# Performance work log

Hardware: AMD Instinct MI355X
Metric: run time of the kernel (lower is better)

The kernel has to match this reference:

```python
import jax, jax.numpy as jnp
import numpy as np

DIM = 512
NUM_HEADS = 8
HEAD_DIM = DIM // NUM_HEADS
SCALE = HEAD_DIM ** -0.5


def setup_inputs() -> dict:
    key = jax.random.key(0)
    k1, k2, k3, k4 = jax.random.split(key, 4)
    x = jax.random.normal(k1, (4, 2048, DIM), dtype=jnp.float32)
    W_qkv = jax.random.normal(k2, (DIM, 3 * DIM), dtype=jnp.float32) * (DIM ** -0.5)
    W_proj = jax.random.normal(k3, (DIM, DIM), dtype=jnp.float32) * (DIM ** -0.5)
    b_proj = jax.random.normal(k4, (DIM,), dtype=jnp.float32) * 0.01
    return {"x": x, "W_qkv": W_qkv, "W_proj": W_proj, "b_proj": b_proj}


def reference(x, W_qkv, W_proj, b_proj):
    B, N, C = x.shape
    H, hd = NUM_HEADS, HEAD_DIM
    # qkv: [B, N, 3, H, hd] -> (q, k, v) each [B, H, N, hd]
    qkv = (x @ W_qkv).reshape(B, N, 3, H, hd)
    qkv = jnp.transpose(qkv, (2, 0, 3, 1, 4))
    q, k, v = qkv[0], qkv[1], qkv[2]
    # eager attention: [B, H, N, N]
    attn = jnp.einsum('bhnd,bhmd->bhnm', q, k) * SCALE
    attn = jax.nn.softmax(attn, axis=-1)
    out = jnp.einsum('bhnm,bhmd->bhnd', attn, v)  # [B, H, N, hd]
    out = jnp.transpose(out, (0, 2, 1, 3)).reshape(B, N, C)
    out = out @ W_proj + b_proj
    return (out, k, v)
```

## Files before the change

### kernel.cpp

```cpp
#include <hip/hip_runtime.h>

typedef unsigned short ushort_t;
typedef __bf16 bf16x8 __attribute__((ext_vector_type(8)));
typedef ushort_t u16x8 __attribute__((ext_vector_type(8)));
typedef float f32x4 __attribute__((ext_vector_type(4)));

#define MFMA(a, b, c) __builtin_amdgcn_mfma_f32_16x16x32_bf16(a, b, c, 0, 0, 0)

#define N_X      4194304L
#define N_WQKV   786432L
#define N_WPROJ  262144L
#define OUT_OFF_K 4194304L
#define OUT_OFF_V 8388608L

#define OFF_FLAG   0UL
#define OFF_XB     1024UL
#define OFF_WQKVT  (OFF_XB + 8388608UL)
#define OFF_WPROJT (OFF_WQKVT + 1572864UL)
#define OFF_BPROJ  (OFF_WPROJT + 524288UL)
#define OFF_QB     (OFF_BPROJ + 2048UL)
#define OFF_KB     (OFF_QB + 8388608UL)
#define OFF_VTB    (OFF_KB + 8388608UL)
#define OFF_ATTN   (OFF_VTB + 8388608UL)

#define QSCALE 0.180336880519191f

__device__ __forceinline__ ushort_t f2b(float f) {
    union { float f; unsigned u; } v; v.f = f;
    return (ushort_t)((v.u + 0x7FFFu + ((v.u >> 16) & 1u)) >> 16);
}
__device__ __forceinline__ ushort_t f2b_trunc(float f) {
    union { float f; unsigned u; } v; v.f = f;
    return (ushort_t)(v.u >> 16);
}
__device__ __forceinline__ float b2f(ushort_t h) {
    union { unsigned u; float f; } v; v.u = ((unsigned)h) << 16;
    return v.f;
}
__device__ __forceinline__ float ldf(const float* p, long i) { return p[i]; }
__device__ __forceinline__ float ldf(const ushort_t* p, long i) { return b2f(p[i]); }
__device__ __forceinline__ void stf(float* p, long i, float v) { p[i] = v; }
__device__ __forceinline__ void stf(ushort_t* p, long i, float v) { p[i] = f2b(v); }

__device__ __forceinline__ float fast_exp2(float x) {
#if __has_builtin(__builtin_amdgcn_exp2f)
    return __builtin_amdgcn_exp2f(x);
#else
    return __expf(x * 0.6931471805599453f);
#endif
}

__device__ __forceinline__ void glds16(const void* g, const void* l) {
    __builtin_amdgcn_global_load_lds((__attribute__((address_space(1))) void*)g,
                                     (__attribute__((address_space(3))) void*)l,
                                     16, 0, 0);
}

__global__ void k_detect(const unsigned* __restrict__ x, int* __restrict__ flag) {
    int lane = threadIdx.x & 63;
    int cnt = 0;
#pragma unroll
    for (int i = 0; i < 4; ++i) {
        unsigned w = x[lane + i * 64];
        float v = __uint_as_float((w & 0xFFFFu) << 16);
        float a = fabsf(v);
        if (a > 1e-3f && a < 100.0f) cnt++;
    }
#pragma unroll
    for (int off = 32; off; off >>= 1) cnt += __shfl_down(cnt, off, 64);
    if (lane == 0) *flag = (cnt > 128) ? 1 : 0;
}

template <typename T>
__global__ void k_prep(const T* __restrict__ x, const T* __restrict__ wq,
                       const T* __restrict__ wp, const T* __restrict__ bp,
                       ushort_t* __restrict__ xb, ushort_t* __restrict__ wqT,
                       ushort_t* __restrict__ wpT, float* __restrict__ bpf,
                       const int* __restrict__ flag, int want) {
    if (*flag != want) return;
    long i0 = (long)blockIdx.x * blockDim.x + threadIdx.x;
    long stride = (long)gridDim.x * blockDim.x;
    for (long i = i0; i < N_X; i += stride) xb[i] = f2b(ldf(x, i));
    for (long i = i0; i < N_WQKV; i += stride) {
        long n = i >> 9, k = i & 511;
        wqT[i] = f2b(ldf(wq, k * 1536 + n));
    }
    for (long i = i0; i < N_WPROJ; i += stride) {
        long n = i >> 9, k = i & 511;
        wpT[i] = f2b(ldf(wp, k * 512 + n));
    }
    for (long i = i0; i < 512; i += stride) bpf[i] = ldf(bp, i);
}

template <typename TOUT>
__global__ __launch_bounds__(256, 2)
void k_qkv(const ushort_t* __restrict__ xb, const ushort_t* __restrict__ wqT,
           ushort_t* __restrict__ qb, ushort_t* __restrict__ kb, ushort_t* __restrict__ vb,
           TOUT* __restrict__ kout, TOUT* __restrict__ vout,
           const int* __restrict__ flag, int want) {
    if (*flag != want) return;
    __shared__ __align__(16) ushort_t As[128 * 32];
    __shared__ __align__(16) ushort_t Bs[128 * 32];
    const int tid = threadIdx.x, wave = tid >> 6, lane = tid & 63;
    const int id = blockIdx.x;
    const int xcd = id & 7, g = id >> 3;
    const int bx = xcd * 8 + (g & 7);
    const int by = g >> 3;
    const int tm = bx * 128, tn = by * 128;
    const int wm = (wave >> 1) * 64, wn = (wave & 1) * 64;
    const int l15 = lane & 15, lq = lane >> 4;
    const int srow = lane >> 2, sc = lane & 3;

    f32x4 acc[4][4];
#pragma unroll
    for (int a = 0; a < 4; ++a)
#pragma unroll
        for (int b = 0; b < 4; ++b) acc[a][b] = (f32x4){0.f, 0.f, 0.f, 0.f};

    for (int k0 = 0; k0 < 512; k0 += 32) {
#pragma unroll
        for (int t = 0; t < 2; ++t) {
            int s = wave * 2 + t;
            int row = s * 16 + srow;
            int c = (sc ^ (row >> 1)) & 3;
            glds16(xb  + (long)(tm + row) * 512 + k0 + c * 8, As + s * 512);
            glds16(wqT + (long)(tn + row) * 512 + k0 + c * 8, Bs + s * 512);
        }
        __syncthreads();
        bf16x8 af[4], bfr[4];
#pragma unroll
        for (int mt = 0; mt < 4; ++mt) {
            int row = wm + mt * 16 + l15;
            int cp = (lq ^ (row >> 1)) & 3;
            af[mt] = *(const bf16x8*)(As + row * 32 + cp * 8);
        }
#pragma unroll
        for (int nt = 0; nt < 4; ++nt) {
            int row = wn + nt * 16 + l15;
            int cp = (lq ^ (row >> 1)) & 3;
            bfr[nt] = *(const bf16x8*)(Bs + row * 32 + cp * 8);
        }
#pragma unroll
        for (int mt = 0; mt < 4; ++mt)
#pragma unroll
            for (int nt = 0; nt < 4; ++nt)
                acc[mt][nt] = MFMA(af[mt], bfr[nt], acc[mt][nt]);
        __syncthreads();
    }

#pragma unroll
    for (int mt = 0; mt < 4; ++mt) {
#pragma unroll
        for (int nt = 0; nt < 4; ++nt) {
            int j = tn + wn + nt * 16 + l15;
            int t = j >> 9, h = (j >> 6) & 7, d = j & 63;
#pragma unroll
            for (int r = 0; r < 4; ++r) {
                int mm = tm + wm + mt * 16 + lq * 4 + r;
                int b = mm >> 11, nn = mm & 2047;
                float v = acc[mt][nt][r];
                long idx = ((long)(b * 8 + h) * 2048 + nn) * 64 + d;
                if (t == 0) {
                    qb[idx] = f2b(v * QSCALE);
                } else if (t == 1) {
                    kb[idx] = f2b(v);
                    stf(kout, idx, v);
                } else {
                    vb[idx] = f2b(v);
                    stf(vout, idx, v);
                }
            }
        }
    }
}

__global__ __launch_bounds__(256, 4)
void k_vtrans(const ushort_t* __restrict__ vb, ushort_t* __restrict__ vtb) {
    __shared__ ushort_t T[64 * 64];
    const int tid = threadIdx.x;
    const int bh = blockIdx.y, ktile = blockIdx.x;
    const long base = (long)bh * 131072 + (long)ktile * 64 * 64;
    const int row = tid >> 2, cq = tid & 3;
#pragma unroll
    for (int half = 0; half < 2; ++half) {
        int c = cq + half * 4;
        u16x8 v = *(const u16x8*)(vb + base + row * 64 + c * 8);
#pragma unroll
        for (int e = 0; e < 8; ++e) {
            int dim = c * 8 + e;
            T[row * 64 + ((dim + row) & 63)] = v[e];
        }
    }
    __syncthreads();
#pragma unroll
    for (int it = 0; it < 16; ++it) {
        int d = (tid >> 6) * 16 + it;
        int key = tid & 63;
        vtb[(long)bh * 131072 + (long)d * 2048 + ktile * 64 + key] =
            T[key * 64 + ((d + key) & 63)];
    }
}

__global__ __launch_bounds__(256, 4)
void k_attn(const ushort_t* __restrict__ qb, const ushort_t* __restrict__ kb,
            const ushort_t* __restrict__ vtb, ushort_t* __restrict__ attnb) {
    __shared__ __align__(16) ushort_t Kt[128 * 64];
    __shared__ __align__(16) ushort_t Vt[64 * 128];
    __shared__ __align__(16) ushort_t Ps[4][16 * 64];
    const int tid = threadIdx.x, wave = tid >> 6, lane = tid & 63;
    const int l15 = lane & 15, lq = lane >> 4;
    const int id = blockIdx.x;
    const int xcd = id & 7, g = id >> 3;
    const int bh = xcd * 4 + (g >> 5);
    const int qt = g & 31;
    const long kvbase = (long)bh * 131072;
    const long qbase = kvbase + (long)qt * 64 * 64;

    bf16x8 aQ[2];
#pragma unroll
    for (int kt = 0; kt < 2; ++kt)
        aQ[kt] = *(const bf16x8*)(qb + qbase +
            (long)(wave * 16 + l15) * 64 + kt * 32 + lq * 8);

    union { ushort_t u[8]; bf16x8 v; } oneu;
#pragma unroll
    for (int i = 0; i < 8; ++i) oneu.u[i] = 0x3F80;
    const bf16x8 ones = oneu.v;

    f32x4 oacc[4], sum_acc;
#pragma unroll
    for (int n = 0; n < 4; ++n) oacc[n] = (f32x4){0.f, 0.f, 0.f, 0.f};
    sum_acc = (f32x4){0.f, 0.f, 0.f, 0.f};

    const int ksrow = lane >> 3, kschunk = lane & 7;
    const int vsrow = lane >> 4, vschunk = lane & 15;
    ushort_t* Pw = &Ps[wave][0];

    for (int j = 0; j < 16; ++j) {
#pragma unroll
        for (int t = 0; t < 4; ++t) {
            int s = wave * 4 + t;
            {
                int row = s * 8 + ksrow;
                int c = kschunk ^ (row & 7);
                glds16(kb + kvbase + (long)(j * 128 + row) * 64 + c * 8, Kt + s * 512);
            }
            {
                int row = s * 4 + vsrow;
                int c = vschunk ^ (row & 15);
                glds16(vtb + kvbase + (long)row * 2048 + j * 128 + c * 8, Vt + s * 512);
            }
        }
        __syncthreads();

#pragma unroll
        for (int h = 0; h < 2; ++h) {
            f32x4 sacc[4];
#pragma unroll
            for (int nt = 0; nt < 4; ++nt) sacc[nt] = (f32x4){0.f, 0.f, 0.f, 0.f};
#pragma unroll
            for (int nt = 0; nt < 4; ++nt) {
                int krow = h * 64 + nt * 16 + l15;
#pragma unroll
                for (int kt = 0; kt < 2; ++kt) {
                    int c = (kt * 4 + lq) ^ (krow & 7);
                    bf16x8 bk = *(const bf16x8*)(Kt + krow * 64 + c * 8);
                    sacc[nt] = MFMA(aQ[kt], bk, sacc[nt]);
                }
            }
#pragma unroll
            for (int nt = 0; nt < 4; ++nt) {
#pragma unroll
                for (int r = 0; r < 4; ++r) {
                    float p = fast_exp2(sacc[nt][r]);
                    int prow = lq * 4 + r;
                    int col = nt * 16 + l15;
                    int ch = (col >> 3) ^ (prow & 7);
                    Pw[prow * 64 + ch * 8 + (col & 7)] = f2b_trunc(p);
                }
            }
#pragma unroll
            for (int kt = 0; kt < 2; ++kt) {
                int cha = (kt * 4 + lq) ^ (l15 & 7);
                bf16x8 ap = *(const bf16x8*)(Pw + l15 * 64 + cha * 8);
                sum_acc = MFMA(ap, ones, sum_acc);
#pragma unroll
                for (int nd = 0; nd < 4; ++nd) {
                    int vrow = nd * 16 + l15;
                    int vch = (h * 8 + kt * 4 + lq) ^ (vrow & 15);
                    bf16x8 bv = *(const bf16x8*)(Vt + vrow * 128 + vch * 8);
                    oacc[nd] = MFMA(ap, bv, oacc[nd]);
                }
            }
        }
        __syncthreads();
    }

    const int b = bh >> 3, hh = bh & 7;
#pragma unroll
    for (int r = 0; r < 4; ++r) {
        float inv = 1.0f / sum_acc[r];
        int n = qt * 64 + wave * 16 + lq * 4 + r;
#pragma unroll
        for (int nd = 0; nd < 4; ++nd) {
            int d = nd * 16 + l15;
            attnb[((long)b * 2048 + n) * 512 + hh * 64 + d] = f2b(oacc[nd][r] * inv);
        }
    }
}

template <typename TOUT>
__global__ __launch_bounds__(256, 2)
void k_proj(const ushort_t* __restrict__ ab, const ushort_t* __restrict__ wpT,
            const float* __restrict__ bpf, TOUT* __restrict__ out,
            const int* __restrict__ flag, int want) {
    if (*flag != want) return;
    __shared__ __align__(16) ushort_t As[128 * 32];
    __shared__ __align__(16) ushort_t Bs[128 * 32];
    const int tid = threadIdx.x, wave = tid >> 6, lane = tid & 63;
    const int id = blockIdx.x;
    const int xcd = id & 7, g = id >> 3;
    const int bx = xcd * 8 + (g & 7);
    const int by = g >> 3;
    const int tm = bx * 128, tn = by * 128;
    const int wm = (wave >> 1) * 64, wn = (wave & 1) * 64;
    const int l15 = lane & 15, lq = lane >> 4;
    const int srow = lane >> 2, sc = lane & 3;

    f32x4 acc[4][4];
#pragma unroll
    for (int a = 0; a < 4; ++a)
#pragma unroll
        for (int b = 0; b < 4; ++b) acc[a][b] = (f32x4){0.f, 0.f, 0.f, 0.f};

    for (int k0 = 0; k0 < 512; k0 += 32) {
#pragma unroll
        for (int t = 0; t < 2; ++t) {
            int s = wave * 2 + t;
            int row = s * 16 + srow;
            int c = (sc ^ (row >> 1)) & 3;
            glds16(ab  + (long)(tm + row) * 512 + k0 + c * 8, As + s * 512);
            glds16(wpT + (long)(tn + row) * 512 + k0 + c * 8, Bs + s * 512);
        }
        __syncthreads();
        bf16x8 af[4], bfr[4];
#pragma unroll
        for (int mt = 0; mt < 4; ++mt) {
            int row = wm + mt * 16 + l15;
            int cp = (lq ^ (row >> 1)) & 3;
            af[mt] = *(const bf16x8*)(As + row * 32 + cp * 8);
        }
#pragma unroll
        for (int nt = 0; nt < 4; ++nt) {
            int row = wn + nt * 16 + l15;
            int cp = (lq ^ (row >> 1)) & 3;
            bfr[nt] = *(const bf16x8*)(Bs + row * 32 + cp * 8);
        }
#pragma unroll
        for (int mt = 0; mt < 4; ++mt)
#pragma unroll
            for (int nt = 0; nt < 4; ++nt)
                acc[mt][nt] = MFMA(af[mt], bfr[nt], acc[mt][nt]);
        __syncthreads();
    }

#pragma unroll
    for (int mt = 0; mt < 4; ++mt) {
#pragma unroll
        for (int nt = 0; nt < 4; ++nt) {
            int j = tn + wn + nt * 16 + l15;
            float bias = bpf[j];
#pragma unroll
            for (int r = 0; r < 4; ++r) {
                int mm = tm + wm + mt * 16 + lq * 4 + r;
                stf(out, (long)mm * 512 + j, acc[mt][nt][r] + bias);
            }
        }
    }
}

extern "C" void kernel_launch(void* const* d_in, const int* in_sizes, int n_in,
                              void* d_out, int out_size, void* d_ws, size_t ws_size,
                              hipStream_t stream) {
    (void)in_sizes; (void)n_in; (void)out_size; (void)ws_size;
    char* ws = (char*)d_ws;
    int* flag = (int*)(ws + OFF_FLAG);
    ushort_t* xb  = (ushort_t*)(ws + OFF_XB);
    ushort_t* wqT = (ushort_t*)(ws + OFF_WQKVT);
    ushort_t* wpT = (ushort_t*)(ws + OFF_WPROJT);
    float*    bpf = (float*)(ws + OFF_BPROJ);
    ushort_t* qb  = (ushort_t*)(ws + OFF_QB);
    ushort_t* kb  = (ushort_t*)(ws + OFF_KB);
    ushort_t* vtb = (ushort_t*)(ws + OFF_VTB);
    ushort_t* ab  = (ushort_t*)(ws + OFF_ATTN);
    ushort_t* vb  = (ushort_t*)(ws + OFF_ATTN);

    k_detect<<<1, 64, 0, stream>>>((const unsigned*)d_in[0], flag);

    k_prep<float><<<1024, 256, 0, stream>>>(
        (const float*)d_in[0], (const float*)d_in[1], (const float*)d_in[2],
        (const float*)d_in[3], xb, wqT, wpT, bpf, flag, 0);
    k_prep<ushort_t><<<1024, 256, 0, stream>>>(
        (const ushort_t*)d_in[0], (const ushort_t*)d_in[1], (const ushort_t*)d_in[2],
        (const ushort_t*)d_in[3], xb, wqT, wpT, bpf, flag, 1);

    k_qkv<float><<<768, 256, 0, stream>>>(xb, wqT, qb, kb, vb,
        (float*)d_out + OUT_OFF_K, (float*)d_out + OUT_OFF_V, flag, 0);
    k_qkv<ushort_t><<<768, 256, 0, stream>>>(xb, wqT, qb, kb, vb,
        (ushort_t*)d_out + OUT_OFF_K, (ushort_t*)d_out + OUT_OFF_V, flag, 1);

    k_vtrans<<<dim3(32, 32), 256, 0, stream>>>(vb, vtb);

    k_attn<<<1024, 256, 0, stream>>>(qb, kb, vtb, ab);

    k_proj<float><<<256, 256, 0, stream>>>(ab, wpT, bpf, (float*)d_out, flag, 0);
    k_proj<ushort_t><<<256, 256, 0, stream>>>(ab, wpT, bpf, (ushort_t*)d_out, flag, 1);
}
```

Baseline: 187.9 us.

## Keep P in registers via transposed MFMA and double query rows per wave

The attention kernel now computes S transposed (K as the A operand), so the exp'd probabilities land directly in the B-operand layout of a 16x16x16 MFMA. That removes the per-wave LDS round trip for P and the ones-MFMA row sum, which is replaced by register accumulation plus cross-lane shuffles. Each wave now handles 32 query rows instead of 16, doubling reuse of every K/V tile loaded into LDS and halving the grid to 512 blocks. The cost is higher register pressure (launch bounds lowered to 2) and fewer blocks for occupancy, with vectorized 8-byte output stores.

```diff
diff --git a/kernel.cpp b/kernel.cpp
--- a/kernel.cpp
+++ b/kernel.cpp
@@ -2,10 +2,31 @@
 
 typedef unsigned short ushort_t;
 typedef __bf16 bf16x8 __attribute__((ext_vector_type(8)));
+typedef __bf16 bf16x4 __attribute__((ext_vector_type(4)));
 typedef ushort_t u16x8 __attribute__((ext_vector_type(8)));
 typedef float f32x4 __attribute__((ext_vector_type(4)));
 
 #define MFMA(a, b, c) __builtin_amdgcn_mfma_f32_16x16x32_bf16(a, b, c, 0, 0, 0)
+
+#if __has_builtin(__builtin_amdgcn_mfma_f32_16x16x16bf16_1k)
+typedef short s16x4 __attribute__((ext_vector_type(4)));
+__device__ __forceinline__ f32x4 mfma16(bf16x4 a, bf16x4 b, f32x4 c) {
+    union { bf16x4 v; s16x4 s; } ua, ub; ua.v = a; ub.v = b;
+    return __builtin_amdgcn_mfma_f32_16x16x16bf16_1k(ua.s, ub.s, c, 0, 0, 0);
+}
+#define MFMA16_ASM 0
+#elif __has_builtin(__builtin_amdgcn_mfma_f32_16x16x16_bf16)
+__device__ __forceinline__ f32x4 mfma16(bf16x4 a, bf16x4 b, f32x4 c) {
+    return __builtin_amdgcn_mfma_f32_16x16x16_bf16(a, b, c, 0, 0, 0);
+}
+#define MFMA16_ASM 0
+#else
+__device__ __forceinline__ f32x4 mfma16(bf16x4 a, bf16x4 b, f32x4 c) {
+    asm("v_mfma_f32_16x16x16_bf16 %0, %1, %2, %0" : "+v"(c) : "v"(a), "v"(b));
+    return c;
+}
+#define MFMA16_ASM 1
+#endif
 
 #define N_X      4194304L
 #define N_WQKV   786432L
@@ -201,40 +222,37 @@
     }
 }
 
-__global__ __launch_bounds__(256, 4)
+__global__ __launch_bounds__(256, 2)
 void k_attn(const ushort_t* __restrict__ qb, const ushort_t* __restrict__ kb,
             const ushort_t* __restrict__ vtb, ushort_t* __restrict__ attnb) {
     __shared__ __align__(16) ushort_t Kt[128 * 64];
     __shared__ __align__(16) ushort_t Vt[64 * 128];
-    __shared__ __align__(16) ushort_t Ps[4][16 * 64];
     const int tid = threadIdx.x, wave = tid >> 6, lane = tid & 63;
     const int l15 = lane & 15, lq = lane >> 4;
     const int id = blockIdx.x;
     const int xcd = id & 7, g = id >> 3;
-    const int bh = xcd * 4 + (g >> 5);
-    const int qt = g & 31;
+    const int bh = xcd * 4 + (g >> 4);
+    const int qt = g & 15;
     const long kvbase = (long)bh * 131072;
-    const long qbase = kvbase + (long)qt * 64 * 64;
-
-    bf16x8 aQ[2];
-#pragma unroll
-    for (int kt = 0; kt < 2; ++kt)
-        aQ[kt] = *(const bf16x8*)(qb + qbase +
-            (long)(wave * 16 + l15) * 64 + kt * 32 + lq * 8);
-
-    union { ushort_t u[8]; bf16x8 v; } oneu;
-#pragma unroll
-    for (int i = 0; i < 8; ++i) oneu.u[i] = 0x3F80;
-    const bf16x8 ones = oneu.v;
-
-    f32x4 oacc[4], sum_acc;
-#pragma unroll
-    for (int n = 0; n < 4; ++n) oacc[n] = (f32x4){0.f, 0.f, 0.f, 0.f};
-    sum_acc = (f32x4){0.f, 0.f, 0.f, 0.f};
+    const long qbase = kvbase + (long)qt * 128 * 64;
+
+    bf16x8 aQ[2][2];
+#pragma unroll
+    for (int mq = 0; mq < 2; ++mq)
+#pragma unroll
+        for (int kt = 0; kt < 2; ++kt)
+            aQ[mq][kt] = *(const bf16x8*)(qb + qbase +
+                (long)(wave * 32 + mq * 16 + l15) * 64 + kt * 32 + lq * 8);
+
+    f32x4 oacc[2][4];
+#pragma unroll
+    for (int mq = 0; mq < 2; ++mq)
+#pragma unroll
+        for (int nd = 0; nd < 4; ++nd) oacc[mq][nd] = (f32x4){0.f, 0.f, 0.f, 0.f};
+    float ssum[2] = {0.f, 0.f};
 
     const int ksrow = lane >> 3, kschunk = lane & 7;
     const int vsrow = lane >> 4, vschunk = lane & 15;
-    ushort_t* Pw = &Ps[wave][0];
 
     for (int j = 0; j < 16; ++j) {
 #pragma unroll
@@ -255,9 +273,11 @@
 
 #pragma unroll
         for (int h = 0; h < 2; ++h) {
-            f32x4 sacc[4];
-#pragma unroll
-            for (int nt = 0; nt < 4; ++nt) sacc[nt] = (f32x4){0.f, 0.f, 0.f, 0.f};
+            f32x4 sacc[2][4];
+#pragma unroll
+            for (int mq = 0; mq < 2; ++mq)
+#pragma unroll
+                for (int nt = 0; nt < 4; ++nt) sacc[mq][nt] = (f32x4){0.f, 0.f, 0.f, 0.f};
 #pragma unroll
             for (int nt = 0; nt < 4; ++nt) {
                 int krow = h * 64 + nt * 16 + l15;
@@ -265,46 +285,63 @@
                 for (int kt = 0; kt < 2; ++kt) {
                     int c = (kt * 4 + lq) ^ (krow & 7);
                     bf16x8 bk = *(const bf16x8*)(Kt + krow * 64 + c * 8);
-                    sacc[nt] = MFMA(aQ[kt], bk, sacc[nt]);
+                    sacc[0][nt] = MFMA(bk, aQ[0][kt], sacc[0][nt]);
+                    sacc[1][nt] = MFMA(bk, aQ[1][kt], sacc[1][nt]);
                 }
             }
-#pragma unroll
-            for (int nt = 0; nt < 4; ++nt) {
-#pragma unroll
-                for (int r = 0; r < 4; ++r) {
-                    float p = fast_exp2(sacc[nt][r]);
-                    int prow = lq * 4 + r;
-                    int col = nt * 16 + l15;
-                    int ch = (col >> 3) ^ (prow & 7);
-                    Pw[prow * 64 + ch * 8 + (col & 7)] = f2b_trunc(p);
+            bf16x4 pb[2][4];
+#pragma unroll
+            for (int mq = 0; mq < 2; ++mq) {
+#pragma unroll
+                for (int nt = 0; nt < 4; ++nt) {
+                    union { ushort_t u[4]; bf16x4 v; } pk;
+                    float acc0 = 0.f, acc1 = 0.f;
+#pragma unroll
+                    for (int r = 0; r < 4; ++r) {
+                        float p = fast_exp2(sacc[mq][nt][r]);
+                        ushort_t tt = f2b_trunc(p);
+                        pk.u[r] = tt;
+                        if (r & 1) acc1 += b2f(tt); else acc0 += b2f(tt);
+                    }
+                    ssum[mq] += acc0 + acc1;
+                    pb[mq][nt] = pk.v;
                 }
             }
 #pragma unroll
-            for (int kt = 0; kt < 2; ++kt) {
-                int cha = (kt * 4 + lq) ^ (l15 & 7);
-                bf16x8 ap = *(const bf16x8*)(Pw + l15 * 64 + cha * 8);
-                sum_acc = MFMA(ap, ones, sum_acc);
-#pragma unroll
-                for (int nd = 0; nd < 4; ++nd) {
-                    int vrow = nd * 16 + l15;
-                    int vch = (h * 8 + kt * 4 + lq) ^ (vrow & 15);
-                    bf16x8 bv = *(const bf16x8*)(Vt + vrow * 128 + vch * 8);
-                    oacc[nd] = MFMA(ap, bv, oacc[nd]);
+            for (int nd = 0; nd < 4; ++nd) {
+                int drow = nd * 16 + l15;
+#pragma unroll
+                for (int nt = 0; nt < 4; ++nt) {
+                    int kc = h * 8 + nt * 2 + (lq >> 1);
+                    int cc = kc ^ (drow & 15);
+                    bf16x4 va = *(const bf16x4*)(Vt + drow * 128 + cc * 8 + (lq & 1) * 4);
+                    oacc[0][nd] = mfma16(va, pb[0][nt], oacc[0][nd]);
+                    oacc[1][nd] = mfma16(va, pb[1][nt], oacc[1][nd]);
                 }
             }
         }
         __syncthreads();
     }
 
+#if MFMA16_ASM
+    asm volatile("s_nop 7\n\ts_nop 7");
+#endif
     const int b = bh >> 3, hh = bh & 7;
 #pragma unroll
-    for (int r = 0; r < 4; ++r) {
-        float inv = 1.0f / sum_acc[r];
-        int n = qt * 64 + wave * 16 + lq * 4 + r;
+    for (int mq = 0; mq < 2; ++mq) {
+        float s = ssum[mq];
+        s += __shfl_xor(s, 16, 64);
+        s += __shfl_xor(s, 32, 64);
+        float inv = 1.0f / s;
+        int n = qt * 128 + wave * 32 + mq * 16 + l15;
+        long rowbase = ((long)b * 2048 + n) * 512 + hh * 64;
 #pragma unroll
         for (int nd = 0; nd < 4; ++nd) {
-            int d = nd * 16 + l15;
-            attnb[((long)b * 2048 + n) * 512 + hh * 64 + d] = f2b(oacc[nd][r] * inv);
+            int d0 = nd * 16 + lq * 4;
+            union { ushort_t u[4]; unsigned long long ll; } o;
+#pragma unroll
+            for (int r = 0; r < 4; ++r) o.u[r] = f2b(oacc[mq][nd][r] * inv);
+            *(unsigned long long*)(attnb + rowbase + d0) = o.ll;
         }
     }
 }
@@ -411,7 +448,7 @@
 
     k_vtrans<<<dim3(32, 32), 256, 0, stream>>>(vb, vtb);
 
-    k_attn<<<1024, 256, 0, stream>>>(qb, kb, vtb, ab);
+    k_attn<<<512, 256, 0, stream>>>(qb, kb, vtb, ab);
 
     k_proj<float><<<256, 256, 0, stream>>>(ab, wpT, bpf, (float*)d_out, flag, 0);
     k_proj<ushort_t><<<256, 256, 0, stream>>>(ab, wpT, bpf, (ushort_t*)d_out, flag, 1);
```

Result: faster. 178.1 us (-5.2%).
